# Optimization experiments

Measured on AMD Instinct MI355X. Metric: run time of the kernel, lower is better.

## Reference

```python
import jax, jax.numpy as jnp
import numpy as np

B, S, D, H = 2, 2048, 1024, 16
HD = D // H  # head dim = 64; scale uses sqrt(d_k/num_heads) = sqrt(D/H) since d_k==d_model


def setup_inputs() -> dict:
    key = jax.random.key(0)
    ks = jax.random.split(key, 12)
    s = 1.0 / np.sqrt(D)
    inp = {
        "Q": jax.random.normal(ks[0], (B, S, D), jnp.float32),
        "K": jax.random.normal(ks[1], (B, S, D), jnp.float32),
        "V": jax.random.normal(ks[2], (B, S, D), jnp.float32),
        "mask": jnp.tril(jnp.ones((S, S), jnp.int32))[None, None],  # [1,1,S,S] causal
        "Wq": jax.random.normal(ks[3], (D, D), jnp.float32) * s,
        "bq": jnp.zeros((D,), jnp.float32),
        "Wk": jax.random.normal(ks[4], (D, D), jnp.float32) * s,
        "bk": jnp.zeros((D,), jnp.float32),
        "Wv": jax.random.normal(ks[5], (D, D), jnp.float32) * s,
        "bv": jnp.zeros((D,), jnp.float32),
        "Wo": jax.random.normal(ks[6], (D, D), jnp.float32) * s,
        "bo": jnp.zeros((D,), jnp.float32),
    }
    return inp


def _split_heads(x):
    # [B,S,D] -> [B,H,S,HD]
    b, s, _ = x.shape
    return x.reshape(b, s, H, HD).transpose(0, 2, 1, 3)


def reference(Q, K, V, mask, Wq, bq, Wk, bk, Wv, bv, Wo, bo):
    q = _split_heads(Q @ Wq.T + bq)
    k = _split_heads(K @ Wk.T + bk)
    v = _split_heads(V @ Wv.T + bv)
    scale = 1.0 / jnp.sqrt(jnp.asarray(D / H, q.dtype))  # d_k/num_heads with d_k=d_model
    scores = jnp.einsum('bhqd,bhkd->bhqk', q, k) * scale
    scores = jnp.where(mask == 0, jnp.asarray(-1e9, scores.dtype), scores)
    probs = jax.nn.softmax(scores, axis=-1)
    z = jnp.einsum('bhqk,bhkd->bhqd', probs, v)  # [B,H,S,HD]
    z = z.transpose(0, 2, 1, 3).reshape(Q.shape[0], Q.shape[1], D)
    return z @ Wo.T + bo
```

## Files before the change

### kernel.cpp

```cpp
#include <hip/hip_runtime.h>
#include <hip/hip_bf16.h>

typedef unsigned short u16;
typedef unsigned int u32;
typedef __attribute__((ext_vector_type(2))) unsigned int u32x2;
typedef __attribute__((ext_vector_type(8))) short s16x8;
typedef __attribute__((ext_vector_type(4))) float f32x4;
typedef __attribute__((ext_vector_type(16))) float f32x16;

#define NB 2
#define NH 16
#define NS 2048
#define ND 1024
#define QSCALE 0.1803368801111244f

#define AS1(p) ((const __attribute__((address_space(1))) void*)(p))
#define AS3(p) ((__attribute__((address_space(3))) void*)(p))

__device__ __forceinline__ u16 f2bf(float f) {
  u32 u = __float_as_uint(f);
  u = u + 0x7FFFu + ((u >> 16) & 1u);
  return (u16)(u >> 16);
}

__device__ __forceinline__ float bf2f(u16 h) {
  return __uint_as_float(((u32)h) << 16);
}

__device__ __forceinline__ u32 pkbf(float a, float b) {
  __hip_bfloat162 h = __float22bfloat162_rn(make_float2(a, b));
  union { __hip_bfloat162 h; u32 u; } cv;
  cv.h = h;
  return cv.u;
}

__global__ __launch_bounds__(256) void cvt_kernel(
    const float* __restrict__ q, const float* __restrict__ k,
    const float* __restrict__ v, const float* __restrict__ wq,
    const float* __restrict__ wk, const float* __restrict__ wv,
    const float* __restrict__ wo, u16* __restrict__ Xbf,
    u16* __restrict__ Wbf) {
  const int s = blockIdx.z;
  const size_t M1 = (size_t)1024 * 1024;
  const float* src;
  u16* dst;
  if (s < 4)       { src = q + (size_t)s * M1;        dst = Xbf + (size_t)s * M1; }
  else if (s < 8)  { src = k + (size_t)(s - 4) * M1;  dst = Xbf + (size_t)s * M1; }
  else if (s < 12) { src = v + (size_t)(s - 8) * M1;  dst = Xbf + (size_t)s * M1; }
  else if (s == 12){ src = wq; dst = Wbf; }
  else if (s == 13){ src = wk; dst = Wbf + M1; }
  else if (s == 14){ src = wv; dst = Wbf + 2 * M1; }
  else             { src = wo; dst = Wbf + 3 * M1; }
  const int n4 = 1024 * 1024 / 4;
  for (int i = blockIdx.x * 256 + threadIdx.x; i < n4; i += gridDim.x * 256) {
    float4 a = ((const float4*)src)[i];
    uint2 p;
    p.x = (u32)f2bf(a.x) | ((u32)f2bf(a.y) << 16);
    p.y = (u32)f2bf(a.z) | ((u32)f2bf(a.w) << 16);
    ((uint2*)dst)[i] = p;
  }
}

__global__ __launch_bounds__(256) void gemm_qkv_fast(
    const u16* __restrict__ Xbf, const u16* __restrict__ Wbf,
    const float* __restrict__ bq, const float* __restrict__ bk,
    const float* __restrict__ bv, u16* __restrict__ qh, u16* __restrict__ kh,
    u16* __restrict__ vT) {
  const int which = blockIdx.z;
  const int m0 = blockIdx.y * 128, n0 = blockIdx.x * 128;
  const u16* A = Xbf + (size_t)which * 4096 * 1024;
  const u16* B = Wbf + (size_t)which * 1024 * 1024;
  const float* bias = (which == 0) ? bq : (which == 1) ? bk : bv;
  const int tid = threadIdx.x;
  const int w = tid >> 6, l = tid & 63, lr = l & 15, lg = l >> 4;
  const int wr = (w >> 1) * 64, wc = (w & 1) * 64;

  __shared__ u16 As[2][128 * 32];
  __shared__ u16 Bs[2][128 * 32];

  const int c0 = tid, c1 = 256 + tid;
  const int row0 = c0 >> 2, k40 = (c0 & 3) ^ (row0 & 3);
  const int row1 = c1 >> 2, k41 = (c1 & 3) ^ (row1 & 3);
  const u16* sa0 = A + (size_t)(m0 + row0) * 1024 + k40 * 8;
  const u16* sb0 = B + (size_t)(n0 + row0) * 1024 + k40 * 8;
  const u16* sa1 = A + (size_t)(m0 + row1) * 1024 + k41 * 8;
  const u16* sb1 = B + (size_t)(n0 + row1) * 1024 + k41 * 8;
  const int d0 = (w * 64) * 8, d1 = (256 + w * 64) * 8;

  const f32x4 fzero = {0.f, 0.f, 0.f, 0.f};
  f32x4 acc[4][4];
#pragma unroll
  for (int m = 0; m < 4; ++m)
#pragma unroll
    for (int n = 0; n < 4; ++n) acc[m][n] = fzero;

  auto STAGE = [&](int buf, int k0) {
    __builtin_amdgcn_global_load_lds(AS1(sa0 + k0), AS3(As[buf] + d0), 16, 0, 0);
    __builtin_amdgcn_global_load_lds(AS1(sb0 + k0), AS3(Bs[buf] + d0), 16, 0, 0);
    __builtin_amdgcn_global_load_lds(AS1(sa1 + k0), AS3(As[buf] + d1), 16, 0, 0);
    __builtin_amdgcn_global_load_lds(AS1(sb1 + k0), AS3(Bs[buf] + d1), 16, 0, 0);
  };

  STAGE(0, 0);
  STAGE(1, 32);
  asm volatile("s_waitcnt vmcnt(4)" ::: "memory");
  __builtin_amdgcn_sched_barrier(0);
  __builtin_amdgcn_s_barrier();

  int cur = 0;
  for (int step = 0; step < 32; ++step) {
    s16x8 af[4], bf[4];
#pragma unroll
    for (int m = 0; m < 4; ++m) {
      int row = wr + m * 16 + lr;
      af[m] = *(const s16x8*)(As[cur] + row * 32 + ((lg ^ (row & 3)) * 8));
    }
#pragma unroll
    for (int n = 0; n < 4; ++n) {
      int row = wc + n * 16 + lr;
      bf[n] = *(const s16x8*)(Bs[cur] + row * 32 + ((lg ^ (row & 3)) * 8));
    }
    asm volatile("s_waitcnt lgkmcnt(0)" ::: "memory");
    __builtin_amdgcn_sched_barrier(0);
    __builtin_amdgcn_s_barrier();

    const bool stg = (step + 2 < 32);
    if (stg) STAGE(cur, (step + 2) * 32);

    __builtin_amdgcn_s_setprio(1);
#pragma unroll
    for (int m = 0; m < 4; ++m)
#pragma unroll
      for (int n = 0; n < 4; ++n)
        acc[m][n] = __builtin_amdgcn_mfma_f32_16x16x32_bf16(af[m], bf[n],
                                                            acc[m][n], 0, 0, 0);
    __builtin_amdgcn_s_setprio(0);

    if (stg)
      asm volatile("s_waitcnt vmcnt(4)" ::: "memory");
    else
      asm volatile("s_waitcnt vmcnt(0)" ::: "memory");
    __builtin_amdgcn_sched_barrier(0);
    __builtin_amdgcn_s_barrier();
    cur ^= 1;
  }

#pragma unroll
  for (int m = 0; m < 4; ++m) {
#pragma unroll
    for (int n = 0; n < 4; ++n) {
#pragma unroll
      for (int i = 0; i < 4; ++i) {
        int row = m0 + wr + m * 16 + 4 * lg + i;
        int col = n0 + wc + n * 16 + lr;
        float val = acc[m][n][i] + bias[col];
        if (which == 0) val *= QSCALE;
        int bbi = row >> 11, ss = row & 2047;
        int hhd = col >> 6, hd = col & 63;
        if (which == 0) {
          qh[(((size_t)bbi * NH + hhd) * NS + ss) * 64 + hd] = f2bf(val);
        } else if (which == 1) {
          kh[(((size_t)bbi * NH + hhd) * NS + ss) * 64 + hd] = f2bf(val);
        } else {
          vT[(((size_t)bbi * NH + hhd) * 64 + hd) * NS + ss] = f2bf(val);
        }
      }
    }
  }
}

__global__ __launch_bounds__(256) void gemm_out_fast(
    const u16* __restrict__ zin, const u16* __restrict__ Wbf,
    const float* __restrict__ bo, float* __restrict__ out) {
  const u16* B = Wbf + (size_t)3 * 1024 * 1024;
  const int m0 = blockIdx.y * 128, n0 = blockIdx.x * 128;
  const int tid = threadIdx.x;
  const int w = tid >> 6, l = tid & 63, lr = l & 15, lg = l >> 4;
  const int wr = (w >> 1) * 64, wc = (w & 1) * 64;

  __shared__ u16 As[2][128 * 32];
  __shared__ u16 Bs[2][128 * 32];

  const int c0 = tid, c1 = 256 + tid;
  const int row0 = c0 >> 2, k40 = (c0 & 3) ^ (row0 & 3);
  const int row1 = c1 >> 2, k41 = (c1 & 3) ^ (row1 & 3);
  const u16* sa0 = zin + (size_t)(m0 + row0) * 1024 + k40 * 8;
  const u16* sb0 = B + (size_t)(n0 + row0) * 1024 + k40 * 8;
  const u16* sa1 = zin + (size_t)(m0 + row1) * 1024 + k41 * 8;
  const u16* sb1 = B + (size_t)(n0 + row1) * 1024 + k41 * 8;
  const int d0 = (w * 64) * 8, d1 = (256 + w * 64) * 8;

  const f32x4 fzero = {0.f, 0.f, 0.f, 0.f};
  f32x4 acc[4][4];
#pragma unroll
  for (int m = 0; m < 4; ++m)
#pragma unroll
    for (int n = 0; n < 4; ++n) acc[m][n] = fzero;

  auto STAGE = [&](int buf, int k0) {
    __builtin_amdgcn_global_load_lds(AS1(sa0 + k0), AS3(As[buf] + d0), 16, 0, 0);
    __builtin_amdgcn_global_load_lds(AS1(sb0 + k0), AS3(Bs[buf] + d0), 16, 0, 0);
    __builtin_amdgcn_global_load_lds(AS1(sa1 + k0), AS3(As[buf] + d1), 16, 0, 0);
    __builtin_amdgcn_global_load_lds(AS1(sb1 + k0), AS3(Bs[buf] + d1), 16, 0, 0);
  };

  STAGE(0, 0);
  STAGE(1, 32);
  asm volatile("s_waitcnt vmcnt(4)" ::: "memory");
  __builtin_amdgcn_sched_barrier(0);
  __builtin_amdgcn_s_barrier();

  int cur = 0;
  for (int step = 0; step < 32; ++step) {
    s16x8 af[4], bf[4];
#pragma unroll
    for (int m = 0; m < 4; ++m) {
      int row = wr + m * 16 + lr;
      af[m] = *(const s16x8*)(As[cur] + row * 32 + ((lg ^ (row & 3)) * 8));
    }
#pragma unroll
    for (int n = 0; n < 4; ++n) {
      int row = wc + n * 16 + lr;
      bf[n] = *(const s16x8*)(Bs[cur] + row * 32 + ((lg ^ (row & 3)) * 8));
    }
    asm volatile("s_waitcnt lgkmcnt(0)" ::: "memory");
    __builtin_amdgcn_sched_barrier(0);
    __builtin_amdgcn_s_barrier();

    const bool stg = (step + 2 < 32);
    if (stg) STAGE(cur, (step + 2) * 32);

    __builtin_amdgcn_s_setprio(1);
#pragma unroll
    for (int m = 0; m < 4; ++m)
#pragma unroll
      for (int n = 0; n < 4; ++n)
        acc[m][n] = __builtin_amdgcn_mfma_f32_16x16x32_bf16(af[m], bf[n],
                                                            acc[m][n], 0, 0, 0);
    __builtin_amdgcn_s_setprio(0);

    if (stg)
      asm volatile("s_waitcnt vmcnt(4)" ::: "memory");
    else
      asm volatile("s_waitcnt vmcnt(0)" ::: "memory");
    __builtin_amdgcn_sched_barrier(0);
    __builtin_amdgcn_s_barrier();
    cur ^= 1;
  }

#pragma unroll
  for (int m = 0; m < 4; ++m)
#pragma unroll
    for (int n = 0; n < 4; ++n)
#pragma unroll
      for (int i = 0; i < 4; ++i) {
        int row = m0 + wr + m * 16 + 4 * lg + i;
        int col = n0 + wc + n * 16 + lr;
        out[(size_t)row * 1024 + col] = acc[m][n][i] + bo[col];
      }
}

__device__ __forceinline__ void stage64(const u16* __restrict__ kh,
                                        const u16* __restrict__ vT, int bh,
                                        int t, int tid, int w, u16* kbase,
                                        u16* vbase) {
#pragma unroll
  for (int i = 0; i < 2; ++i) {
    int c = i * 256 + tid;
    int row = c >> 3, k8 = (c & 7) ^ (row & 7);
    const u16* sk = kh + ((size_t)bh * NS + t * 64 + row) * 64 + k8 * 8;
    const u16* sv = vT + ((size_t)bh * 64 + row) * NS + t * 64 + k8 * 8;
    u16* dk = kbase + (i * 256 + w * 64) * 8;
    u16* dv = vbase + (i * 256 + w * 64) * 8;
    __builtin_amdgcn_global_load_lds(AS1(sk), AS3(dk), 16, 0, 0);
    __builtin_amdgcn_global_load_lds(AS1(sv), AS3(dv), 16, 0, 0);
  }
}

__global__ __launch_bounds__(256) void attn_split_kernel(
    const u16* __restrict__ qh, const u16* __restrict__ kh,
    const u16* __restrict__ vT, u16* __restrict__ Opart,
    float* __restrict__ Mpart, float* __restrict__ Lpart) {
  const int f = blockIdx.x;
  const int bh = f & 31;
  const int pp = f >> 5;
  const int tid = threadIdx.x;
  const int w = tid >> 6, l = tid & 63;
  const int ql = l & 31, hi = l >> 5, hi8 = hi * 8;

  __shared__ u16 smem[2][2][64][64];

#pragma unroll 1
  for (int c = 0; c < 2; ++c) {
    const int band = c ? (15 - pp) : pp;
    const int t0 = c ? (16 - pp) : 0;
    const int t1 = c ? (32 - 2 * pp) : (pp + 1);
    const int q0w = band * 128 + w * 32;

    s16x8 qf[4];
    {
      const u16* qp = qh + ((size_t)bh * NS + q0w + ql) * 64 + hi8;
#pragma unroll
      for (int st = 0; st < 4; ++st) qf[st] = *(const s16x8*)(qp + st * 16);
    }

    f32x16 o0 = {0, 0, 0, 0, 0, 0, 0, 0, 0, 0, 0, 0, 0, 0, 0, 0};
    f32x16 o1 = {0, 0, 0, 0, 0, 0, 0, 0, 0, 0, 0, 0, 0, 0, 0, 0};
    float m_run = -1e30f, l_run = 0.f;

    __syncthreads();
    stage64(kh, vT, bh, t0, tid, w, &smem[t0 & 1][0][0][0],
            &smem[t0 & 1][1][0][0]);
    __syncthreads();

    for (int t = t0; t < t1; ++t) {
      if (t + 1 < t1)
        stage64(kh, vT, bh, t + 1, tid, w, &smem[(t + 1) & 1][0][0][0],
                &smem[(t + 1) & 1][1][0][0]);
      const u16* kp = &smem[t & 1][0][0][0];
      const u16* vp = &smem[t & 1][1][0][0];

      const int kvg0 = t * 64, kvg1 = t * 64 + 32;
      if (kvg0 <= q0w) {
        f32x16 s0 = {0, 0, 0, 0, 0, 0, 0, 0, 0, 0, 0, 0, 0, 0, 0, 0};
        f32x16 s1 = {0, 0, 0, 0, 0, 0, 0, 0, 0, 0, 0, 0, 0, 0, 0, 0};
        const int kr0 = ql, kr1 = 32 + ql;
        __builtin_amdgcn_s_setprio(1);
#pragma unroll
        for (int st = 0; st < 4; ++st) {
          s16x8 ak = *(const s16x8*)(kp + kr0 * 64 +
                                     (((st * 2 + hi) ^ (kr0 & 7)) * 8));
          s0 = __builtin_amdgcn_mfma_f32_32x32x16_bf16(ak, qf[st], s0, 0, 0, 0);
        }
        if (kvg1 <= q0w) {
#pragma unroll
          for (int st = 0; st < 4; ++st) {
            s16x8 ak = *(const s16x8*)(kp + kr1 * 64 +
                                       (((st * 2 + hi) ^ (kr1 & 7)) * 8));
            s1 = __builtin_amdgcn_mfma_f32_32x32x16_bf16(ak, qf[st], s1, 0, 0,
                                                         0);
          }
        }
        __builtin_amdgcn_s_setprio(0);

        if (kvg0 == q0w) {
#pragma unroll
          for (int r = 0; r < 16; ++r) {
            int kvloc = (r & 3) + 8 * (r >> 2) + 4 * hi;
            if (kvloc > ql) s0[r] = -1e30f;
          }
        }
        if (kvg1 > q0w) {
#pragma unroll
          for (int r = 0; r < 16; ++r) s1[r] = -1e30f;
        } else if (kvg1 == q0w) {
#pragma unroll
          for (int r = 0; r < 16; ++r) {
            int kvloc = (r & 3) + 8 * (r >> 2) + 4 * hi;
            if (kvloc > ql) s1[r] = -1e30f;
          }
        }

        float mr[16];
#pragma unroll
        for (int r = 0; r < 16; ++r) mr[r] = fmaxf(s0[r], s1[r]);
#pragma unroll
        for (int off = 8; off; off >>= 1)
#pragma unroll
          for (int r = 0; r < 8; ++r)
            if (r < off) mr[r] = fmaxf(mr[r], mr[r + off]);
        float mx = mr[0];
        {
          u32x2 rm = __builtin_amdgcn_permlane32_swap(
              __float_as_uint(mx), __float_as_uint(mx), 0, 0);
          mx = fmaxf(__uint_as_float(rm.x), __uint_as_float(rm.y));
        }

        if (!__all(mx - m_run <= 8.0f)) {
          float mnew = fmaxf(m_run, mx);
          float fs = __builtin_amdgcn_exp2f(m_run - mnew);
#pragma unroll
          for (int r = 0; r < 16; ++r) {
            o0[r] *= fs;
            o1[r] *= fs;
          }
          l_run *= fs;
          m_run = mnew;
        }

        float ps = 0.f;
        u32 pk0[8], pk1[8];
#pragma unroll
        for (int tt = 0; tt < 8; ++tt) {
          float a = __builtin_amdgcn_exp2f(s0[2 * tt] - m_run);
          float b = __builtin_amdgcn_exp2f(s0[2 * tt + 1] - m_run);
          ps += a + b;
          pk0[tt] = pkbf(a, b);
        }
#pragma unroll
        for (int tt = 0; tt < 8; ++tt) {
          float a = __builtin_amdgcn_exp2f(s1[2 * tt] - m_run);
          float b = __builtin_amdgcn_exp2f(s1[2 * tt + 1] - m_run);
          ps += a + b;
          pk1[tt] = pkbf(a, b);
        }
        {
          u32x2 rp = __builtin_amdgcn_permlane32_swap(
              __float_as_uint(ps), __float_as_uint(ps), 0, 0);
          ps = __uint_as_float(rp.x) + __uint_as_float(rp.y);
        }
        l_run += ps;

        u32x2 e0 = __builtin_amdgcn_permlane32_swap(pk0[0], pk0[2], 0, 0);
        u32x2 e1 = __builtin_amdgcn_permlane32_swap(pk0[1], pk0[3], 0, 0);
        u32x2 e2 = __builtin_amdgcn_permlane32_swap(pk0[4], pk0[6], 0, 0);
        u32x2 e3 = __builtin_amdgcn_permlane32_swap(pk0[5], pk0[7], 0, 0);
        u32x2 e4 = __builtin_amdgcn_permlane32_swap(pk1[0], pk1[2], 0, 0);
        u32x2 e5 = __builtin_amdgcn_permlane32_swap(pk1[1], pk1[3], 0, 0);
        u32x2 e6 = __builtin_amdgcn_permlane32_swap(pk1[4], pk1[6], 0, 0);
        u32x2 e7 = __builtin_amdgcn_permlane32_swap(pk1[5], pk1[7], 0, 0);
        union { u32 u[4]; s16x8 h; } pf[4];
        pf[0].u[0] = e0.x; pf[0].u[1] = e1.x; pf[0].u[2] = e0.y; pf[0].u[3] = e1.y;
        pf[1].u[0] = e2.x; pf[1].u[1] = e3.x; pf[1].u[2] = e2.y; pf[1].u[3] = e3.y;
        pf[2].u[0] = e4.x; pf[2].u[1] = e5.x; pf[2].u[2] = e4.y; pf[2].u[3] = e5.y;
        pf[3].u[0] = e6.x; pf[3].u[1] = e7.x; pf[3].u[2] = e6.y; pf[3].u[3] = e7.y;

        __builtin_amdgcn_s_setprio(1);
#pragma unroll
        for (int ks = 0; ks < 4; ++ks) {
          int ch = ks * 2 + hi;
          s16x8 av0 = *(const s16x8*)(vp + ql * 64 + ((ch ^ (ql & 7)) * 8));
          s16x8 av1 =
              *(const s16x8*)(vp + (32 + ql) * 64 + ((ch ^ (ql & 7)) * 8));
          o0 = __builtin_amdgcn_mfma_f32_32x32x16_bf16(av0, pf[ks].h, o0, 0, 0,
                                                       0);
          o1 = __builtin_amdgcn_mfma_f32_32x32x16_bf16(av1, pf[ks].h, o1, 0, 0,
                                                       0);
        }
        __builtin_amdgcn_s_setprio(0);
      }
      __syncthreads();
    }

    u16* Zw = &smem[0][0][0][0] + w * (32 * 72);
#pragma unroll
    for (int r = 0; r < 16; r += 2) {
      int d0 = (r & 3) + 8 * (r >> 2) + 4 * hi;
      *(u32*)&Zw[ql * 72 + d0]      = pkbf(o0[r], o0[r + 1]);
      *(u32*)&Zw[ql * 72 + 32 + d0] = pkbf(o1[r], o1[r + 1]);
    }
    if (hi == 0) {
      size_t mix = ((size_t)c * 32 + bh) * NS + q0w + ql;
      Mpart[mix] = m_run;
      Lpart[mix] = l_run;
    }
#pragma unroll
    for (int i = 0; i < 4; ++i) {
      int cid = i * 64 + l;
      int row = cid >> 3, c8 = (cid & 7) * 8;
      s16x8 vv = *(const s16x8*)&Zw[row * 72 + c8];
      *(s16x8*)(Opart + (((size_t)c * 32 + bh) * NS + q0w + row) * 64 + c8) =
          vv;
    }
  }
}

__global__ __launch_bounds__(256) void attn_combine_kernel(
    const u16* __restrict__ Opart, const float* __restrict__ Mpart,
    const float* __restrict__ Lpart, u16* __restrict__ z) {
  const int tok = blockIdx.x;
  const int bb = tok >> 11, ss = tok & 2047;
  const int t = threadIdx.x;
  const int d4 = t * 4;
  const int hh = d4 >> 6;
  const size_t qix = ((size_t)bb * NH + hh) * NS + ss;
  const size_t stride = (size_t)32 * NS;

  float m0 = Mpart[qix], l0 = Lpart[qix];
  float m1 = Mpart[qix + stride], l1 = Lpart[qix + stride];
  float mm = fmaxf(m0, m1);
  float w0 = __builtin_amdgcn_exp2f(m0 - mm);
  float w1 = __builtin_amdgcn_exp2f(m1 - mm);
  float inv = 1.f / (w0 * l0 + w1 * l1);
  w0 *= inv;
  w1 *= inv;

  size_t ob = qix * 64 + (d4 & 63);
  uint2 a = *(const uint2*)(Opart + ob);
  uint2 b = *(const uint2*)(Opart + ob + stride * 64);

  float z0 = bf2f((u16)(a.x & 0xffff)) * w0 + bf2f((u16)(b.x & 0xffff)) * w1;
  float z1 = bf2f((u16)(a.x >> 16)) * w0 + bf2f((u16)(b.x >> 16)) * w1;
  float z2 = bf2f((u16)(a.y & 0xffff)) * w0 + bf2f((u16)(b.y & 0xffff)) * w1;
  float z3 = bf2f((u16)(a.y >> 16)) * w0 + bf2f((u16)(b.y >> 16)) * w1;

  uint2 p;
  p.x = pkbf(z0, z1);
  p.y = pkbf(z2, z3);
  *(uint2*)(z + ((size_t)bb * NS + ss) * ND + d4) = p;
}

__global__ __launch_bounds__(128) void attn_kernel(
    const u16* __restrict__ qh, const u16* __restrict__ kh,
    const u16* __restrict__ vT, u16* __restrict__ z) {
  const int f = blockIdx.x;
  const int bh = f & 31;
  const int j0 = (f >> 5) & 7;
  const int g = f >> 8;
  const int mb = 2 * j0;
  const int m =
      (g == 0) ? mb : (g == 1) ? mb + 1 : (g == 2) ? 30 - mb : 31 - mb;
  const int bb = bh >> 4, hh = bh & 15;
  const int tid = threadIdx.x;
  const int w = tid >> 6, l = tid & 63;
  const int ql = l & 31, hi = l >> 5, hi8 = hi * 8;
  const int q0w = m * 64 + w * 32;

  __shared__ u16 smem[2][2][64][64];

  s16x8 qf[4];
  {
    const u16* qp = qh + ((size_t)bh * NS + q0w + ql) * 64 + hi8;
#pragma unroll
    for (int st = 0; st < 4; ++st) qf[st] = *(const s16x8*)(qp + st * 16);
  }

  f32x16 o0 = {0, 0, 0, 0, 0, 0, 0, 0, 0, 0, 0, 0, 0, 0, 0, 0};
  f32x16 o1 = {0, 0, 0, 0, 0, 0, 0, 0, 0, 0, 0, 0, 0, 0, 0, 0};
  float m_run = -1e30f, l_run = 0.f;

  const int ntiles = m + 1;

#pragma unroll
  for (int i = 0; i < 4; ++i) {
    int c = i * 128 + tid;
    int row = c >> 3, k8 = (c & 7) ^ (row & 7);
    const u16* sk = kh + ((size_t)bh * NS + row) * 64 + k8 * 8;
    const u16* sv = vT + ((size_t)bh * 64 + row) * NS + k8 * 8;
    u16* dk = &smem[0][0][0][0] + (i * 128 + w * 64) * 8;
    u16* dv = &smem[0][1][0][0] + (i * 128 + w * 64) * 8;
    __builtin_amdgcn_global_load_lds(AS1(sk), AS3(dk), 16, 0, 0);
    __builtin_amdgcn_global_load_lds(AS1(sv), AS3(dv), 16, 0, 0);
  }
  __syncthreads();

  for (int t = 0; t < ntiles; ++t) {
    if (t + 1 < ntiles) {
      int b1 = (t + 1) & 1;
#pragma unroll
      for (int i = 0; i < 4; ++i) {
        int c = i * 128 + tid;
        int row = c >> 3, k8 = (c & 7) ^ (row & 7);
        const u16* sk =
            kh + ((size_t)bh * NS + (t + 1) * 64 + row) * 64 + k8 * 8;
        const u16* sv =
            vT + ((size_t)bh * 64 + row) * NS + (t + 1) * 64 + k8 * 8;
        u16* dk = &smem[b1][0][0][0] + (i * 128 + w * 64) * 8;
        u16* dv = &smem[b1][1][0][0] + (i * 128 + w * 64) * 8;
        __builtin_amdgcn_global_load_lds(AS1(sk), AS3(dk), 16, 0, 0);
        __builtin_amdgcn_global_load_lds(AS1(sv), AS3(dv), 16, 0, 0);
      }
    }
    const u16* kp = &smem[t & 1][0][0][0];
    const u16* vp = &smem[t & 1][1][0][0];

#pragma unroll
    for (int sub = 0; sub < 2; ++sub) {
      const int kvg = t * 64 + sub * 32;
      if (kvg > q0w) continue;
      const bool masked = (kvg == q0w);

      const int kr = sub * 32 + ql;
      f32x16 s = {0, 0, 0, 0, 0, 0, 0, 0, 0, 0, 0, 0, 0, 0, 0, 0};
#pragma unroll
      for (int st = 0; st < 4; ++st) {
        s16x8 ak = *(const s16x8*)(kp + kr * 64 +
                                   (((st * 2 + hi) ^ (kr & 7)) * 8));
        s = __builtin_amdgcn_mfma_f32_32x32x16_bf16(ak, qf[st], s, 0, 0, 0);
      }

      float sv_[16];
#pragma unroll
      for (int r = 0; r < 16; ++r) {
        float x = s[r];
        if (masked) {
          int kvloc = (r & 3) + 8 * (r >> 2) + 4 * hi;
          if (kvloc > ql) x = -1e30f;
        }
        sv_[r] = x;
      }

      float mx = sv_[0];
#pragma unroll
      for (int r = 1; r < 16; ++r) mx = fmaxf(mx, sv_[r]);
      {
        u32x2 rm = __builtin_amdgcn_permlane32_swap(__float_as_uint(mx),
                                                    __float_as_uint(mx), 0, 0);
        mx = fmaxf(__uint_as_float(rm.x), __uint_as_float(rm.y));
      }

      if (__any(mx > m_run)) {
        float mnew = fmaxf(m_run, mx);
        float fs = __builtin_amdgcn_exp2f(m_run - mnew);
#pragma unroll
        for (int r = 0; r < 16; ++r) {
          o0[r] *= fs;
          o1[r] *= fs;
        }
        l_run *= fs;
        m_run = mnew;
      }

      float ps = 0.f;
      u32 pk[8];
#pragma unroll
      for (int tt = 0; tt < 8; ++tt) {
        float a = __builtin_amdgcn_exp2f(sv_[2 * tt] - m_run);
        float b = __builtin_amdgcn_exp2f(sv_[2 * tt + 1] - m_run);
        ps += a + b;
        pk[tt] = pkbf(a, b);
      }
      {
        u32x2 rp = __builtin_amdgcn_permlane32_swap(__float_as_uint(ps),
                                                    __float_as_uint(ps), 0, 0);
        ps = __uint_as_float(rp.x) + __uint_as_float(rp.y);
      }
      l_run += ps;

      u32x2 e0 = __builtin_amdgcn_permlane32_swap(pk[0], pk[2], 0, 0);
      u32x2 e1 = __builtin_amdgcn_permlane32_swap(pk[1], pk[3], 0, 0);
      u32x2 e2 = __builtin_amdgcn_permlane32_swap(pk[4], pk[6], 0, 0);
      u32x2 e3 = __builtin_amdgcn_permlane32_swap(pk[5], pk[7], 0, 0);
      union { u32 u[4]; s16x8 h; } pf0, pf1;
      pf0.u[0] = e0.x; pf0.u[1] = e1.x; pf0.u[2] = e0.y; pf0.u[3] = e1.y;
      pf1.u[0] = e2.x; pf1.u[1] = e3.x; pf1.u[2] = e2.y; pf1.u[3] = e3.y;

#pragma unroll
      for (int k2 = 0; k2 < 2; ++k2) {
        s16x8 pa = (k2 == 0) ? pf0.h : pf1.h;
        int ch = sub * 4 + k2 * 2 + hi;
        s16x8 av0 = *(const s16x8*)(vp + ql * 64 + ((ch ^ (ql & 7)) * 8));
        s16x8 av1 =
            *(const s16x8*)(vp + (32 + ql) * 64 + ((ch ^ (ql & 7)) * 8));
        o0 = __builtin_amdgcn_mfma_f32_32x32x16_bf16(av0, pa, o0, 0, 0, 0);
        o1 = __builtin_amdgcn_mfma_f32_32x32x16_bf16(av1, pa, o1, 0, 0, 0);
      }
    }
    __syncthreads();
  }

  float inv = 1.f / l_run;
  u16* Zw = &smem[0][0][0][0] + w * (32 * 72);
#pragma unroll
  for (int r = 0; r < 16; r += 2) {
    int d0 = (r & 3) + 8 * (r >> 2) + 4 * hi;
    *(u32*)&Zw[ql * 72 + d0]      = pkbf(o0[r] * inv, o0[r + 1] * inv);
    *(u32*)&Zw[ql * 72 + 32 + d0] = pkbf(o1[r] * inv, o1[r + 1] * inv);
  }
#pragma unroll
  for (int i = 0; i < 4; ++i) {
    int cid = i * 64 + l;
    int row = cid >> 3, c8 = (cid & 7) * 8;
    s16x8 vv = *(const s16x8*)&Zw[row * 72 + c8];
    *(s16x8*)(z + ((size_t)bb * NS + q0w + row) * ND + hh * 64 + c8) = vv;
  }
}

__global__ __launch_bounds__(256) void proj_qkv_kernel(
    const float* __restrict__ Qin, const float* __restrict__ Kin,
    const float* __restrict__ Vin,
    const float* __restrict__ Wq, const float* __restrict__ bq,
    const float* __restrict__ Wk, const float* __restrict__ bk,
    const float* __restrict__ Wv, const float* __restrict__ bv,
    u16* __restrict__ qh, u16* __restrict__ kh, u16* __restrict__ vT) {
  const int which = blockIdx.z;
  const float* X = (which == 0) ? Qin : (which == 1) ? Kin : Vin;
  const float* W = (which == 0) ? Wq : (which == 1) ? Wk : Wv;
  const float* bias = (which == 0) ? bq : (which == 1) ? bk : bv;

  const int m0 = blockIdx.y * 128, n0 = blockIdx.x * 128;
  const int tid = threadIdx.x;
  const int w = tid >> 6, l = tid & 63, lr = l & 15, lg = l >> 4;
  const int wr = (w >> 1) * 64, wc = (w & 1) * 64;

  __shared__ u16 As[128][40];
  __shared__ u16 Bs[128][40];

  const f32x4 fzero = {0.f, 0.f, 0.f, 0.f};
  f32x4 acc[4][4];
#pragma unroll
  for (int m = 0; m < 4; ++m)
#pragma unroll
    for (int n = 0; n < 4; ++n) acc[m][n] = fzero;

  for (int k0 = 0; k0 < 1024; k0 += 32) {
#pragma unroll
    for (int i = 0; i < 4; ++i) {
      int idx = tid + i * 256;
      int row = idx >> 3, c4 = (idx & 7) * 4;
      float4 a = *(const float4*)(X + (size_t)(m0 + row) * 1024 + k0 + c4);
      *(u32*)&As[row][c4]     = (u32)f2bf(a.x) | ((u32)f2bf(a.y) << 16);
      *(u32*)&As[row][c4 + 2] = (u32)f2bf(a.z) | ((u32)f2bf(a.w) << 16);
      float4 b = *(const float4*)(W + (size_t)(n0 + row) * 1024 + k0 + c4);
      *(u32*)&Bs[row][c4]     = (u32)f2bf(b.x) | ((u32)f2bf(b.y) << 16);
      *(u32*)&Bs[row][c4 + 2] = (u32)f2bf(b.z) | ((u32)f2bf(b.w) << 16);
    }
    __syncthreads();
    s16x8 af[4], bf[4];
#pragma unroll
    for (int m = 0; m < 4; ++m)
      af[m] = *(const s16x8*)&As[wr + m * 16 + lr][lg * 8];
#pragma unroll
    for (int n = 0; n < 4; ++n)
      bf[n] = *(const s16x8*)&Bs[wc + n * 16 + lr][lg * 8];
#pragma unroll
    for (int m = 0; m < 4; ++m)
#pragma unroll
      for (int n = 0; n < 4; ++n)
        acc[m][n] = __builtin_amdgcn_mfma_f32_16x16x32_bf16(af[m], bf[n],
                                                            acc[m][n], 0, 0, 0);
    __syncthreads();
  }

  u16* dst01 = (which == 0) ? qh : kh;
#pragma unroll
  for (int m = 0; m < 4; ++m) {
#pragma unroll
    for (int n = 0; n < 4; ++n) {
#pragma unroll
      for (int i = 0; i < 4; ++i) {
        int row = m0 + wr + m * 16 + 4 * lg + i;
        int col = n0 + wc + n * 16 + lr;
        float val = acc[m][n][i] + bias[col];
        if (which == 0) val *= QSCALE;
        int bbi = row >> 11, ss = row & 2047;
        int hhd = col >> 6, hd = col & 63;
        if (which < 2) {
          dst01[(((size_t)bbi * NH + hhd) * NS + ss) * 64 + hd] = f2bf(val);
        } else {
          vT[(((size_t)bbi * NH + hhd) * 64 + hd) * NS + ss] = f2bf(val);
        }
      }
    }
  }
}

__global__ __launch_bounds__(256) void proj_out_kernel(
    const u16* __restrict__ zin, const float* __restrict__ Wo,
    const float* __restrict__ bo, float* __restrict__ out) {
  const int m0 = blockIdx.y * 128, n0 = blockIdx.x * 128;
  const int tid = threadIdx.x;
  const int w = tid >> 6, l = tid & 63, lr = l & 15, lg = l >> 4;
  const int wr = (w >> 1) * 64, wc = (w & 1) * 64;

  __shared__ u16 As[128][40];
  __shared__ u16 Bs[128][40];

  const f32x4 fzero = {0.f, 0.f, 0.f, 0.f};
  f32x4 acc[4][4];
#pragma unroll
  for (int m = 0; m < 4; ++m)
#pragma unroll
    for (int n = 0; n < 4; ++n) acc[m][n] = fzero;

  for (int k0 = 0; k0 < 1024; k0 += 32) {
#pragma unroll
    for (int i = 0; i < 2; ++i) {
      int idx = tid + i * 256;
      int row = idx >> 2, c8 = (idx & 3) * 8;
      *(s16x8*)&As[row][c8] =
          *(const s16x8*)(zin + (size_t)(m0 + row) * 1024 + k0 + c8);
    }
#pragma unroll
    for (int i = 0; i < 4; ++i) {
      int idx = tid + i * 256;
      int row = idx >> 3, c4 = (idx & 7) * 4;
      float4 b = *(const float4*)(Wo + (size_t)(n0 + row) * 1024 + k0 + c4);
      *(u32*)&Bs[row][c4]     = (u32)f2bf(b.x) | ((u32)f2bf(b.y) << 16);
      *(u32*)&Bs[row][c4 + 2] = (u32)f2bf(b.z) | ((u32)f2bf(b.w) << 16);
    }
    __syncthreads();
    s16x8 af[4], bf[4];
#pragma unroll
    for (int m = 0; m < 4; ++m)
      af[m] = *(const s16x8*)&As[wr + m * 16 + lr][lg * 8];
#pragma unroll
    for (int n = 0; n < 4; ++n)
      bf[n] = *(const s16x8*)&Bs[wc + n * 16 + lr][lg * 8];
#pragma unroll
    for (int m = 0; m < 4; ++m)
#pragma unroll
      for (int n = 0; n < 4; ++n)
        acc[m][n] = __builtin_amdgcn_mfma_f32_16x16x32_bf16(af[m], bf[n],
                                                            acc[m][n], 0, 0, 0);
    __syncthreads();
  }

#pragma unroll
  for (int m = 0; m < 4; ++m)
#pragma unroll
    for (int n = 0; n < 4; ++n)
#pragma unroll
      for (int i = 0; i < 4; ++i) {
        int row = m0 + wr + m * 16 + 4 * lg + i;
        int col = n0 + wc + n * 16 + lr;
        out[(size_t)row * 1024 + col] = acc[m][n][i] + bo[col];
      }
}

extern "C" void kernel_launch(void* const* d_in, const int* in_sizes, int n_in,
                              void* d_out, int out_size, void* d_ws,
                              size_t ws_size, hipStream_t stream) {
  const float* Q = (const float*)d_in[0];
  const float* K = (const float*)d_in[1];
  const float* V = (const float*)d_in[2];
  const float* Wq = (const float*)d_in[4];
  const float* bq = (const float*)d_in[5];
  const float* Wk = (const float*)d_in[6];
  const float* bk = (const float*)d_in[7];
  const float* Wv = (const float*)d_in[8];
  const float* bv = (const float*)d_in[9];
  const float* Wo = (const float*)d_in[10];
  const float* bo = (const float*)d_in[11];
  float* out = (float*)d_out;

  const size_t M1 = (size_t)1024 * 1024;
  u16* base = (u16*)d_ws;

  if (ws_size >= (size_t)58720256) {
    u16* Wbf = base;
    u16* qh = base + 4 * M1;
    u16* zz = qh;
    u16* kh = base + 8 * M1;
    u16* vT = base + 12 * M1;
    u16* Xbf = base + 16 * M1;
    u16* Opart = base + 16 * M1;
    float* Mpart = (float*)(base + 24 * M1);
    float* Lpart = (float*)(base + 24 * M1 + 256 * 1024);

    cvt_kernel<<<dim3(128, 1, 16), 256, 0, stream>>>(Q, K, V, Wq, Wk, Wv, Wo,
                                                     Xbf, Wbf);
    gemm_qkv_fast<<<dim3(8, 32, 3), 256, 0, stream>>>(Xbf, Wbf, bq, bk, bv,
                                                      qh, kh, vT);
    attn_split_kernel<<<dim3(512), 256, 0, stream>>>(qh, kh, vT, Opart, Mpart,
                                                     Lpart);
    attn_combine_kernel<<<dim3(4096), 256, 0, stream>>>(Opart, Mpart, Lpart,
                                                        zz);
    gemm_out_fast<<<dim3(8, 32), 256, 0, stream>>>(zz, Wbf, bo, out);
  } else {
    u16* qh = base;
    u16* kh = base + 4 * M1;
    u16* vT = base + 8 * M1;
    u16* zz = base + 12 * M1;
    proj_qkv_kernel<<<dim3(8, 32, 3), 256, 0, stream>>>(Q, K, V, Wq, bq, Wk,
                                                        bk, Wv, bv, qh, kh, vT);
    attn_kernel<<<dim3(1024), 128, 0, stream>>>(qh, kh, vT, zz);
    proj_out_kernel<<<dim3(8, 32), 256, 0, stream>>>(zz, Wo, bo, out);
  }
}
```

Measured before the change: 132.6 us.

## Triple-buffer K/V tiles in attention with partial vmcnt waits

Grows the shared K/V staging buffer from two to three slots and prefetches two tiles ahead using async global-to-LDS loads. The end-of-iteration __syncthreads is replaced by an explicit s_waitcnt vmcnt(4) plus s_barrier, so the wait covers only the tile needed next and the newer prefetch stays in flight. This is meant to hide global load latency behind MFMA work. In exchange it uses more LDS, which may reduce occupancy, and it relies on the count of 4 outstanding loads per stage being exact.

```diff
diff --git a/kernel.cpp b/kernel.cpp
--- a/kernel.cpp
+++ b/kernel.cpp
@@ -288,13 +288,14 @@
   const int w = tid >> 6, l = tid & 63;
   const int ql = l & 31, hi = l >> 5, hi8 = hi * 8;
 
-  __shared__ u16 smem[2][2][64][64];
+  __shared__ u16 smem[3][2][64][64];
 
 #pragma unroll 1
   for (int c = 0; c < 2; ++c) {
     const int band = c ? (15 - pp) : pp;
     const int t0 = c ? (16 - pp) : 0;
     const int t1 = c ? (32 - 2 * pp) : (pp + 1);
+    const int nt = t1 - t0;
     const int q0w = band * 128 + w * 32;
 
     s16x8 qf[4];
@@ -309,16 +310,25 @@
     float m_run = -1e30f, l_run = 0.f;
 
     __syncthreads();
-    stage64(kh, vT, bh, t0, tid, w, &smem[t0 & 1][0][0][0],
-            &smem[t0 & 1][1][0][0]);
-    __syncthreads();
+    stage64(kh, vT, bh, t0, tid, w, &smem[t0 % 3][0][0][0],
+            &smem[t0 % 3][1][0][0]);
+    if (nt > 1)
+      stage64(kh, vT, bh, t0 + 1, tid, w, &smem[(t0 + 1) % 3][0][0][0],
+              &smem[(t0 + 1) % 3][1][0][0]);
+    if (nt > 1)
+      asm volatile("s_waitcnt vmcnt(4)" ::: "memory");
+    else
+      asm volatile("s_waitcnt vmcnt(0)" ::: "memory");
+    __builtin_amdgcn_sched_barrier(0);
+    __builtin_amdgcn_s_barrier();
 
     for (int t = t0; t < t1; ++t) {
-      if (t + 1 < t1)
-        stage64(kh, vT, bh, t + 1, tid, w, &smem[(t + 1) & 1][0][0][0],
-                &smem[(t + 1) & 1][1][0][0]);
-      const u16* kp = &smem[t & 1][0][0][0];
-      const u16* vp = &smem[t & 1][1][0][0];
+      const bool stg = (t + 2 < t1);
+      if (stg)
+        stage64(kh, vT, bh, t + 2, tid, w, &smem[(t + 2) % 3][0][0][0],
+                &smem[(t + 2) % 3][1][0][0]);
+      const u16* kp = &smem[t % 3][0][0][0];
+      const u16* vp = &smem[t % 3][1][0][0];
 
       const int kvg0 = t * 64, kvg1 = t * 64 + 32;
       if (kvg0 <= q0w) {
@@ -439,7 +449,13 @@
         }
         __builtin_amdgcn_s_setprio(0);
       }
-      __syncthreads();
+
+      if (stg)
+        asm volatile("s_waitcnt vmcnt(4)" ::: "memory");
+      else
+        asm volatile("s_waitcnt vmcnt(0)" ::: "memory");
+      __builtin_amdgcn_sched_barrier(0);
+      __builtin_amdgcn_s_barrier();
     }
 
     u16* Zw = &smem[0][0][0][0] + w * (32 * 72);
```

After: 134.1 us. About the same (+1.1%).
